# Performance work log

Measured on AMD Instinct MI355X. Metric: run time of the kernel, lower is better.

## Reference

```python
import jax, jax.numpy as jnp
import numpy as np

NHEAD = 16
HEAD_DIM = 64
EMBED_DIM = NHEAD * HEAD_DIM  # 1024
U, R, L, M = 2048, 256, 1024, 512


def setup_inputs() -> dict:
    key = jax.random.key(0)
    ks = jax.random.split(key, 11)
    D = EMBED_DIM
    inp = {
        "utterance": jax.random.normal(ks[0], (U, 1, D), jnp.float32),
        "right_context": jax.random.normal(ks[1], (R, 1, D), jnp.float32),
        "memory": jax.random.normal(ks[2], (M, 1, D), jnp.float32),
        "left_context_key": jax.random.normal(ks[3], (L, 1, D), jnp.float32),
        "left_context_val": jax.random.normal(ks[4], (L, 1, D), jnp.float32),
        "Wq": jax.random.normal(ks[5], (D, D), jnp.float32) * 0.02,
        "bq": jax.random.normal(ks[6], (D,), jnp.float32) * 0.02,
        "Wkv": jax.random.normal(ks[7], (2 * D, D), jnp.float32) * 0.02,
        "bkv": jax.random.normal(ks[8], (2 * D,), jnp.float32) * 0.02,
        "Wo": jax.random.normal(ks[9], (D, D), jnp.float32) * 0.02,
        "bo": jax.random.normal(ks[10], (D,), jnp.float32) * 0.02,
    }
    return inp


def reference(utterance, right_context, memory, left_context_key, left_context_val,
              Wq, bq, Wkv, bkv, Wo, bo):
    D = EMBED_DIM
    scaling = HEAD_DIM ** (-0.5)

    # query = Linear([right_context; utterance])  -> (Q, 1, D), Q = R + U
    q_in = jnp.concatenate([right_context, utterance], axis=0)
    query = q_in @ Wq.T + bq

    # key/value = Linear([memory; right_context; utterance]) split in two
    kv_in = jnp.concatenate([memory, right_context, utterance], axis=0)
    kv = kv_in @ Wkv.T + bkv  # (M+R+U, 1, 2D)
    k_new, v_new = kv[..., :D], kv[..., D:]

    # insert cached left-context key/value after [memory; right_context]
    key = jnp.concatenate([k_new[: M + R], left_context_key, k_new[M + R:]], axis=0)
    value = jnp.concatenate([v_new[: M + R], left_context_val, v_new[M + R:]], axis=0)

    Q = U + R
    KV = M + R + L + U
    # (T, 1, D) -> (nhead, T, head_dim)
    q = query.reshape(Q, NHEAD, HEAD_DIM).transpose(1, 0, 2)
    k = key.reshape(KV, NHEAD, HEAD_DIM).transpose(1, 0, 2)
    v = value.reshape(KV, NHEAD, HEAD_DIM).transpose(1, 0, 2)

    weights = jnp.einsum("hqd,hkd->hqk", q * scaling, k)  # (nhead, Q, KV)
    probs = jax.nn.softmax(weights, axis=-1)
    attn = jnp.einsum("hqk,hkd->hqd", probs, v)  # (nhead, Q, head_dim)

    attn = attn.transpose(1, 0, 2).reshape(Q, D)[:, None, :]  # (Q, 1, D)
    out = attn @ Wo.T + bo
    return out, key, value
```

## Files before the change

### kernel.cpp

```cpp
#include <hip/hip_runtime.h>
#include <hip/hip_bf16.h>

#define EMBED   1024
#define NHEADS  16
#define HDIM    64
#define U_LEN   2048
#define R_LEN   256
#define L_LEN   1024
#define M_LEN   512
#define Q_LEN   (U_LEN + R_LEN)
#define KV_LEN  (M_LEN + R_LEN + L_LEN + U_LEN)
#define X_ROWS  (M_LEN + R_LEN + U_LEN)
#define NPART   3
#define KV_PART (KV_LEN / NPART)

typedef __attribute__((ext_vector_type(8))) short short8;
typedef __attribute__((ext_vector_type(4))) float f32x4;
typedef __attribute__((ext_vector_type(16))) float f32x16;

#define QSCALE 0.180336880f

__device__ __forceinline__ void gl2lds16(const __hip_bfloat16* g, __hip_bfloat16* l) {
  __builtin_amdgcn_global_load_lds(
      (const __attribute__((address_space(1))) unsigned int*)g,
      (__attribute__((address_space(3))) unsigned int*)l, 16, 0, 0);
}

__device__ __forceinline__ unsigned pack_bf16(float a, float b) {
  unsigned r;
  asm("v_cvt_pk_bf16_f32 %0, %1, %2" : "=v"(r) : "v"(a), "v"(b));
  return r;
}

__device__ __forceinline__ void plane_swap(unsigned a, unsigned b, int h2,
                                           unsigned& lo, unsigned& hi) {
#if __has_builtin(__builtin_amdgcn_permlane32_swap)
  auto r = __builtin_amdgcn_permlane32_swap(a, b, false, false);
  lo = r[0]; hi = r[1];
#else
  unsigned s0 = h2 ? a : b;
  unsigned r0 = __shfl_xor(s0, 32, 64);
  lo = h2 ? r0 : a;
  hi = h2 ? b : r0;
#endif
}

__global__ __launch_bounds__(256) void prep_kernel(
    const float* __restrict__ mem, const float* __restrict__ rc,
    const float* __restrict__ utt, const float* __restrict__ lk,
    const float* __restrict__ lv, const float* __restrict__ Wq,
    const float* __restrict__ Wkv, const float* __restrict__ Wo,
    __hip_bfloat16* __restrict__ X, __hip_bfloat16* __restrict__ WB,
    __hip_bfloat16* __restrict__ WoB,
    float* __restrict__ key_out, float* __restrict__ val_out,
    __hip_bfloat16* __restrict__ k_bf, __hip_bfloat16* __restrict__ v_bf) {
  int b = blockIdx.x, tid = threadIdx.x;
  if (b < 2816) {
    int row = b, col = tid * 4;
    const float* src;
    if (row < M_LEN)              src = mem + row * EMBED;
    else if (row < M_LEN + R_LEN) src = rc + (row - M_LEN) * EMBED;
    else                          src = utt + (row - M_LEN - R_LEN) * EMBED;
    float4 v = *reinterpret_cast<const float4*>(src + col);
    uint2 pk; pk.x = pack_bf16(v.x, v.y); pk.y = pack_bf16(v.z, v.w);
    *reinterpret_cast<uint2*>(X + (size_t)row * EMBED + col) = pk;
  } else if (b < 6912) {
    const float* src; __hip_bfloat16* dst;
    int blk;
    if (b < 3840)      { src = Wq;  dst = WB;                blk = b - 2816; }
    else if (b < 5888) { src = Wkv; dst = WB + 1024 * 1024;  blk = b - 3840; }
    else               { src = Wo;  dst = WoB;               blk = b - 5888; }
    int idx = blk * 1024 + tid * 4;
    float4 v = *reinterpret_cast<const float4*>(src + idx);
    uint2 pk; pk.x = pack_bf16(v.x, v.y); pk.y = pack_bf16(v.z, v.w);
    *reinterpret_cast<uint2*>(dst + idx) = pk;
  } else {
    int row = b - 6912, c0 = tid * 4;
    int orow = 768 + row;
    float4 kv4 = *reinterpret_cast<const float4*>(lk + row * EMBED + c0);
    float4 vv4 = *reinterpret_cast<const float4*>(lv + row * EMBED + c0);
    *reinterpret_cast<float4*>(key_out + (size_t)orow * EMBED + c0) = kv4;
    *reinterpret_cast<float4*>(val_out + (size_t)orow * EMBED + c0) = vv4;
    uint2 pk, pv;
    pk.x = pack_bf16(kv4.x, kv4.y); pk.y = pack_bf16(kv4.z, kv4.w);
    pv.x = pack_bf16(vv4.x, vv4.y); pv.y = pack_bf16(vv4.z, vv4.w);
    *reinterpret_cast<uint2*>(k_bf + (size_t)orow * EMBED + c0) = pk;
    *reinterpret_cast<uint2*>(v_bf + (size_t)orow * EMBED + c0) = pv;
  }
}

__global__ __launch_bounds__(256) void transpose_kernel(
    const unsigned short* __restrict__ v_bf, unsigned short* __restrict__ vT) {
  __shared__ unsigned short T[64][72];
  int kt = blockIdx.x * 64, d0 = blockIdx.y * 64;
  int t = threadIdx.x;
  int r = t >> 3, c = (t & 7) * 8;
#pragma unroll
  for (int half = 0; half < 2; half++) {
    int kv = r + half * 32;
    short8 v = *reinterpret_cast<const short8*>(v_bf + (size_t)(kt + kv) * EMBED + d0 + c);
#pragma unroll
    for (int j = 0; j < 8; j++) T[c + j][kv] = (unsigned short)v[j];
  }
  __syncthreads();
#pragma unroll
  for (int half = 0; half < 2; half++) {
    int d = r + half * 32;
    *reinterpret_cast<short8*>(vT + (size_t)(d0 + d) * KV_LEN + kt + c) =
        *reinterpret_cast<const short8*>(&T[d][c]);
  }
}

__global__ __launch_bounds__(512) void gemm_qkv(
    const __hip_bfloat16* __restrict__ A, const __hip_bfloat16* __restrict__ B,
    const float* __restrict__ bq, const float* __restrict__ bkv,
    float* __restrict__ key_out, float* __restrict__ val_out,
    __hip_bfloat16* __restrict__ q_bf, __hip_bfloat16* __restrict__ k_bf,
    __hip_bfloat16* __restrict__ v_bf) {
  __shared__ __align__(16) __hip_bfloat16 As[128 * 64];
  __shared__ __align__(16) __hip_bfloat16 Bs[128 * 64];
  const int K = EMBED;
  int tid = threadIdx.x;
  int wave = tid >> 6, lane = tid & 63, quad = lane >> 4, l16 = lane & 15;
  int wm = wave >> 2, wn = wave & 3;
  int mbase = blockIdx.y * 128, nbase = blockIdx.x * 128;

  if (nbase + 128 <= 1024 && mbase + 128 <= 512) return;

  int srow = tid >> 3;
  int scol = ((tid & 7) ^ (srow & 7)) * 8;
  const __hip_bfloat16* aG = A + (size_t)(mbase + srow) * K + scol;
  const __hip_bfloat16* bG = B + (size_t)(nbase + srow) * K + scol;
  int swz = l16 & 7;

  f32x4 acc[4][2] = {};
  for (int kt = 0; kt < K; kt += 64) {
    gl2lds16(aG + kt, As + tid * 8);
    gl2lds16(aG + (size_t)64 * K + kt, As + (tid + 512) * 8);
    gl2lds16(bG + kt, Bs + tid * 8);
    gl2lds16(bG + (size_t)64 * K + kt, Bs + (tid + 512) * 8);
    __syncthreads();
#pragma unroll
    for (int ks = 0; ks < 2; ks++) {
      short8 af[4], bfr[2];
#pragma unroll
      for (int i = 0; i < 4; i++)
        af[i] = *reinterpret_cast<const short8*>(
            As + (wm * 64 + i * 16 + l16) * 64 + ((ks * 4 + quad) ^ swz) * 8);
#pragma unroll
      for (int j = 0; j < 2; j++)
        bfr[j] = *reinterpret_cast<const short8*>(
            Bs + (wn * 32 + j * 16 + l16) * 64 + ((ks * 4 + quad) ^ swz) * 8);
#pragma unroll
      for (int i = 0; i < 4; i++)
#pragma unroll
        for (int j = 0; j < 2; j++)
          acc[i][j] = __builtin_amdgcn_mfma_f32_16x16x32_bf16(af[i], bfr[j], acc[i][j], 0, 0, 0);
    }
    __syncthreads();
  }

#pragma unroll
  for (int i = 0; i < 4; i++) {
    int rb = mbase + wm * 64 + i * 16 + quad * 4;
#pragma unroll
    for (int j = 0; j < 2; j++) {
      int cg = nbase + wn * 32 + j * 16 + l16;
      float bv = (cg < 1024) ? bq[cg] : bkv[cg - 1024];
#pragma unroll
      for (int reg = 0; reg < 4; reg++) {
        int rg = rb + reg;
        float val = acc[i][j][reg] + bv;
        if (cg < 1024) {
          if (rg >= 512)
            q_bf[(size_t)(rg - 512) * 1024 + cg] = __float2bfloat16(val * QSCALE);
        } else {
          int orow = (rg < 768) ? rg : rg + 1024;
          if (cg < 2048) {
            int cc = cg - 1024;
            key_out[(size_t)orow * 1024 + cc] = val;
            k_bf[(size_t)orow * 1024 + cc] = __float2bfloat16(val);
          } else {
            int cc = cg - 2048;
            val_out[(size_t)orow * 1024 + cc] = val;
            v_bf[(size_t)orow * 1024 + cc] = __float2bfloat16(val);
          }
        }
      }
    }
  }
}

__global__ __launch_bounds__(256) void gemm_out(
    const __hip_bfloat16* __restrict__ A, const __hip_bfloat16* __restrict__ B,
    const float* __restrict__ bias, float* __restrict__ outf) {
  __shared__ __align__(16) __hip_bfloat16 As[64 * 64];
  __shared__ __align__(16) __hip_bfloat16 Bs[64 * 64];
  const int K = EMBED, N = EMBED;
  int tid = threadIdx.x;
  int wave = tid >> 6, lane = tid & 63, quad = lane >> 4, l16 = lane & 15;
  int wm = wave >> 1, wn = wave & 1;

  int lid = blockIdx.x;
  int gsw = (lid & 7) * 72 + (lid >> 3);
  int bx = gsw / 36, by = gsw % 36;
  int mbase = by * 64, nbase = bx * 64;

  int srow = tid >> 3;
  int scol = ((tid & 7) ^ (srow & 7)) * 8;
  const __hip_bfloat16* aG = A + (size_t)(mbase + srow) * K + scol;
  const __hip_bfloat16* bG = B + (size_t)(nbase + srow) * K + scol;
  int swz = l16 & 7;

  f32x4 acc[2][2] = {};
  for (int kt = 0; kt < K; kt += 64) {
    gl2lds16(aG + kt, As + tid * 8);
    gl2lds16(aG + (size_t)32 * K + kt, As + (tid + 256) * 8);
    gl2lds16(bG + kt, Bs + tid * 8);
    gl2lds16(bG + (size_t)32 * K + kt, Bs + (tid + 256) * 8);
    __syncthreads();
#pragma unroll
    for (int ks = 0; ks < 2; ks++) {
      short8 af[2], bfr[2];
#pragma unroll
      for (int i = 0; i < 2; i++)
        af[i] = *reinterpret_cast<const short8*>(
            As + (wm * 32 + i * 16 + l16) * 64 + ((ks * 4 + quad) ^ swz) * 8);
#pragma unroll
      for (int j = 0; j < 2; j++)
        bfr[j] = *reinterpret_cast<const short8*>(
            Bs + (wn * 32 + j * 16 + l16) * 64 + ((ks * 4 + quad) ^ swz) * 8);
#pragma unroll
      for (int i = 0; i < 2; i++)
#pragma unroll
        for (int j = 0; j < 2; j++)
          acc[i][j] = __builtin_amdgcn_mfma_f32_16x16x32_bf16(af[i], bfr[j], acc[i][j], 0, 0, 0);
    }
    __syncthreads();
  }

#pragma unroll
  for (int i = 0; i < 2; i++) {
    int rb = mbase + wm * 32 + i * 16 + quad * 4;
#pragma unroll
    for (int j = 0; j < 2; j++) {
      int cg = nbase + wn * 32 + j * 16 + l16;
      float bv = bias[cg];
#pragma unroll
      for (int reg = 0; reg < 4; reg++)
        outf[(size_t)(rb + reg) * N + cg] = acc[i][j][reg] + bv;
    }
  }
}

__global__ __launch_bounds__(256, 4) void attn_kernel(
    const __hip_bfloat16* __restrict__ q_bf, const __hip_bfloat16* __restrict__ k_bf,
    const __hip_bfloat16* __restrict__ vT,
    __hip_bfloat16* __restrict__ o_part, float* __restrict__ lsum) {
  __shared__ __align__(16) __hip_bfloat16 Ks[128][72];
  __shared__ __align__(16) __hip_bfloat16 VTs[64][136];
  int tid = threadIdx.x;
  int w = tid >> 6, lane = tid & 63, l31 = lane & 31, h2 = lane >> 5;

  int lid = blockIdx.x;
  int xcd = lid & 7, sfl = lid >> 3;
  int gi = sfl / 18, j = sfl - gi * 18;
  int g = gi * 8 + xcd;
  int part = g >> 4, h = g & 15;
  int qbase = j * 128;
  int qg = qbase + w * 32 + l31;

  short8 Qf[4];
#pragma unroll
  for (int ks = 0; ks < 4; ks++)
    Qf[ks] = *reinterpret_cast<const short8*>(
        q_bf + (size_t)qg * EMBED + h * HDIM + ks * 16 + h2 * 8);

  f32x16 ot[2] = {};
  float l_run = 0.f;

  int krow = tid >> 3, kcol = (tid & 7) * 8;
  int vrow = tid >> 4, vcol = (tid & 15) * 8;
  const int kv0 = part * KV_PART;

  short8 kr[4], vr[4];
#pragma unroll
  for (int v = 0; v < 4; v++) {
    kr[v] = *reinterpret_cast<const short8*>(
        k_bf + (size_t)(kv0 + v * 32 + krow) * EMBED + h * HDIM + kcol);
    vr[v] = *reinterpret_cast<const short8*>(
        vT + (size_t)(h * HDIM + v * 16 + vrow) * KV_LEN + kv0 + vcol);
  }

  for (int kt = kv0; kt < kv0 + KV_PART; kt += 128) {
    __syncthreads();
#pragma unroll
    for (int v = 0; v < 4; v++) {
      *reinterpret_cast<short8*>(&Ks[v * 32 + krow][kcol]) = kr[v];
      *reinterpret_cast<short8*>(&VTs[v * 16 + vrow][vcol]) = vr[v];
    }
    __syncthreads();
    if (kt + 128 < kv0 + KV_PART) {
#pragma unroll
      for (int v = 0; v < 4; v++) {
        kr[v] = *reinterpret_cast<const short8*>(
            k_bf + (size_t)(kt + 128 + v * 32 + krow) * EMBED + h * HDIM + kcol);
        vr[v] = *reinterpret_cast<const short8*>(
            vT + (size_t)(h * HDIM + v * 16 + vrow) * KV_LEN + kt + 128 + vcol);
      }
    }

#pragma unroll
    for (int kvs = 0; kvs < 4; kvs++) {
      f32x16 s = {};
      __builtin_amdgcn_s_setprio(1);
#pragma unroll
      for (int ks = 0; ks < 4; ks++) {
        short8 ak = *reinterpret_cast<const short8*>(&Ks[kvs * 32 + l31][ks * 16 + h2 * 8]);
        s = __builtin_amdgcn_mfma_f32_32x32x16_bf16(ak, Qf[ks], s, 0, 0, 0);
      }
      __builtin_amdgcn_s_setprio(0);
      unsigned u[4][2];
#pragma unroll
      for (int gq = 0; gq < 4; gq++) {
        float p0 = __builtin_amdgcn_exp2f(s[4 * gq + 0]);
        float p1 = __builtin_amdgcn_exp2f(s[4 * gq + 1]);
        float p2 = __builtin_amdgcn_exp2f(s[4 * gq + 2]);
        float p3 = __builtin_amdgcn_exp2f(s[4 * gq + 3]);
        l_run += (p0 + p1) + (p2 + p3);
        u[gq][0] = pack_bf16(p0, p1);
        u[gq][1] = pack_bf16(p2, p3);
      }
#pragma unroll
      for (int half = 0; half < 2; half++) {
        int c = kvs * 2 + half;
        int gA = 2 * half, gB = 2 * half + 1;
        uint4 fr;
        plane_swap(u[gA][0], u[gB][0], h2, fr.x, fr.z);
        plane_swap(u[gA][1], u[gB][1], h2, fr.y, fr.w);
        short8 pf = __builtin_bit_cast(short8, fr);
        __builtin_amdgcn_s_setprio(1);
#pragma unroll
        for (int ds = 0; ds < 2; ds++) {
          short8 av = *reinterpret_cast<const short8*>(&VTs[ds * 32 + l31][c * 16 + h2 * 8]);
          ot[ds] = __builtin_amdgcn_mfma_f32_32x32x16_bf16(av, pf, ot[ds], 0, 0, 0);
        }
        __builtin_amdgcn_s_setprio(0);
      }
    }
  }

  l_run += __shfl_xor(l_run, 32, 64);
  float inv = 1.0f / l_run;

  size_t orow = (size_t)part * Q_LEN + qg;
#pragma unroll
  for (int ds = 0; ds < 2; ds++)
#pragma unroll
    for (int gq = 0; gq < 4; gq++) {
      uint2 pk;
      pk.x = pack_bf16(ot[ds][4 * gq + 0] * inv, ot[ds][4 * gq + 1] * inv);
      pk.y = pack_bf16(ot[ds][4 * gq + 2] * inv, ot[ds][4 * gq + 3] * inv);
      *reinterpret_cast<uint2*>(
          o_part + orow * 1024 + h * HDIM + ds * 32 + gq * 8 + h2 * 4) = pk;
    }
  if (lane < 32)
    lsum[orow * NHEADS + h] = l_run;
}

__global__ __launch_bounds__(256) void merge_kernel(
    const __hip_bfloat16* __restrict__ o_part, const float* __restrict__ lsum,
    __hip_bfloat16* __restrict__ attn_bf) {
  int q = blockIdx.x;
  int c = threadIdx.x * 4;
  int h = c >> 6;
  float wt[NPART], L = 0.f;
#pragma unroll
  for (int p = 0; p < NPART; p++) {
    wt[p] = lsum[((size_t)p * Q_LEN + q) * NHEADS + h];
    L += wt[p];
  }
  float invL = 1.0f / L;
  float acc[4] = {0.f, 0.f, 0.f, 0.f};
#pragma unroll
  for (int p = 0; p < NPART; p++) {
    __hip_bfloat16 v[4];
    *reinterpret_cast<uint2*>(v) =
        *reinterpret_cast<const uint2*>(o_part + ((size_t)p * Q_LEN + q) * 1024 + c);
#pragma unroll
    for (int jj = 0; jj < 4; jj++) acc[jj] += wt[p] * __bfloat162float(v[jj]);
  }
  uint2 pk;
  pk.x = pack_bf16(acc[0] * invL, acc[1] * invL);
  pk.y = pack_bf16(acc[2] * invL, acc[3] * invL);
  *reinterpret_cast<uint2*>(attn_bf + (size_t)q * 1024 + c) = pk;
}


extern "C" void kernel_launch(void* const* d_in, const int* in_sizes, int n_in,
                              void* d_out, int out_size, void* d_ws, size_t ws_size,
                              hipStream_t stream) {
  const float* utt = (const float*)d_in[0];
  const float* rc  = (const float*)d_in[1];
  const float* mem = (const float*)d_in[2];
  const float* lk  = (const float*)d_in[3];
  const float* lv  = (const float*)d_in[4];
  const float* Wq  = (const float*)d_in[5];
  const float* bq  = (const float*)d_in[6];
  const float* Wkv = (const float*)d_in[7];
  const float* bkv = (const float*)d_in[8];
  const float* Wo  = (const float*)d_in[9];
  const float* bo  = (const float*)d_in[10];

  float* out_f   = (float*)d_out;
  float* key_out = out_f + Q_LEN * EMBED;
  float* val_out = key_out + KV_LEN * EMBED;

  char* ws = (char*)d_ws;
  size_t off = 0;
  __hip_bfloat16* X_bf   = (__hip_bfloat16*)(ws + off); off += (size_t)X_ROWS * EMBED * 2;
  __hip_bfloat16* WB_bf  = (__hip_bfloat16*)(ws + off); off += (size_t)3 * EMBED * EMBED * 2;
  __hip_bfloat16* Wo_bf  = (__hip_bfloat16*)(ws + off); off += (size_t)EMBED * EMBED * 2;
  __hip_bfloat16* q_bf   = (__hip_bfloat16*)(ws + off); off += (size_t)Q_LEN * EMBED * 2;
  __hip_bfloat16* k_bf   = (__hip_bfloat16*)(ws + off); off += (size_t)KV_LEN * EMBED * 2;
  __hip_bfloat16* vT_bf  = (__hip_bfloat16*)(ws + off); off += (size_t)EMBED * KV_LEN * 2;
  __hip_bfloat16* o_part = (__hip_bfloat16*)(ws + off); off += (size_t)NPART * Q_LEN * EMBED * 2;
  __hip_bfloat16* attn_bf = X_bf;
  float* lsum = (float*)WB_bf;
  __hip_bfloat16* v_bf = o_part;
  (void)off; (void)ws_size; (void)in_sizes; (void)n_in; (void)out_size;

  prep_kernel<<<7936, 256, 0, stream>>>(mem, rc, utt, lk, lv, Wq, Wkv, Wo,
                                        X_bf, WB_bf, Wo_bf,
                                        key_out, val_out, k_bf, v_bf);
  gemm_qkv<<<dim3(3 * EMBED / 128, X_ROWS / 128), 512, 0, stream>>>(
      X_bf, WB_bf, bq, bkv, key_out, val_out, q_bf, k_bf, v_bf);
  transpose_kernel<<<dim3(KV_LEN / 64, EMBED / 64), 256, 0, stream>>>(
      (const unsigned short*)v_bf, (unsigned short*)vT_bf);
  attn_kernel<<<dim3((Q_LEN / 128) * NHEADS * NPART), 256, 0, stream>>>(
      q_bf, k_bf, vT_bf, o_part, lsum);
  merge_kernel<<<Q_LEN, 256, 0, stream>>>(o_part, lsum, attn_bf);
  gemm_out<<<576, 256, 0, stream>>>(attn_bf, Wo_bf, bo, out_f);
}
```

Baseline: 200.8 us.

## Fuse V transpose into QKV GEMM epilogue and prep kernel

```diff
diff --git a/kernel.cpp b/kernel.cpp
--- a/kernel.cpp
+++ b/kernel.cpp
@@ -53,7 +53,7 @@
     __hip_bfloat16* __restrict__ X, __hip_bfloat16* __restrict__ WB,
     __hip_bfloat16* __restrict__ WoB,
     float* __restrict__ key_out, float* __restrict__ val_out,
-    __hip_bfloat16* __restrict__ k_bf, __hip_bfloat16* __restrict__ v_bf) {
+    __hip_bfloat16* __restrict__ k_bf, __hip_bfloat16* __restrict__ vT) {
   int b = blockIdx.x, tid = threadIdx.x;
   if (b < 2816) {
     int row = b, col = tid * 4;
@@ -74,40 +74,25 @@
     float4 v = *reinterpret_cast<const float4*>(src + idx);
     uint2 pk; pk.x = pack_bf16(v.x, v.y); pk.y = pack_bf16(v.z, v.w);
     *reinterpret_cast<uint2*>(dst + idx) = pk;
-  } else {
+  } else if (b < 7936) {
     int row = b - 6912, c0 = tid * 4;
     int orow = 768 + row;
     float4 kv4 = *reinterpret_cast<const float4*>(lk + row * EMBED + c0);
     float4 vv4 = *reinterpret_cast<const float4*>(lv + row * EMBED + c0);
     *reinterpret_cast<float4*>(key_out + (size_t)orow * EMBED + c0) = kv4;
     *reinterpret_cast<float4*>(val_out + (size_t)orow * EMBED + c0) = vv4;
-    uint2 pk, pv;
+    uint2 pk;
     pk.x = pack_bf16(kv4.x, kv4.y); pk.y = pack_bf16(kv4.z, kv4.w);
-    pv.x = pack_bf16(vv4.x, vv4.y); pv.y = pack_bf16(vv4.z, vv4.w);
     *reinterpret_cast<uint2*>(k_bf + (size_t)orow * EMBED + c0) = pk;
-    *reinterpret_cast<uint2*>(v_bf + (size_t)orow * EMBED + c0) = pv;
-  }
-}
-
-__global__ __launch_bounds__(256) void transpose_kernel(
-    const unsigned short* __restrict__ v_bf, unsigned short* __restrict__ vT) {
-  __shared__ unsigned short T[64][72];
-  int kt = blockIdx.x * 64, d0 = blockIdx.y * 64;
-  int t = threadIdx.x;
-  int r = t >> 3, c = (t & 7) * 8;
-#pragma unroll
-  for (int half = 0; half < 2; half++) {
-    int kv = r + half * 32;
-    short8 v = *reinterpret_cast<const short8*>(v_bf + (size_t)(kt + kv) * EMBED + d0 + c);
-#pragma unroll
-    for (int j = 0; j < 8; j++) T[c + j][kv] = (unsigned short)v[j];
-  }
-  __syncthreads();
-#pragma unroll
-  for (int half = 0; half < 2; half++) {
-    int d = r + half * 32;
-    *reinterpret_cast<short8*>(vT + (size_t)(d0 + d) * KV_LEN + kt + c) =
-        *reinterpret_cast<const short8*>(&T[d][c]);
+  } else {
+    int d = b - 7936;
+    int kv = tid * 4;
+    float v0 = lv[(size_t)(kv + 0) * EMBED + d];
+    float v1 = lv[(size_t)(kv + 1) * EMBED + d];
+    float v2 = lv[(size_t)(kv + 2) * EMBED + d];
+    float v3 = lv[(size_t)(kv + 3) * EMBED + d];
+    uint2 pk; pk.x = pack_bf16(v0, v1); pk.y = pack_bf16(v2, v3);
+    *reinterpret_cast<uint2*>(vT + (size_t)d * KV_LEN + 768 + kv) = pk;
   }
 }
 
@@ -116,7 +101,7 @@
     const float* __restrict__ bq, const float* __restrict__ bkv,
     float* __restrict__ key_out, float* __restrict__ val_out,
     __hip_bfloat16* __restrict__ q_bf, __hip_bfloat16* __restrict__ k_bf,
-    __hip_bfloat16* __restrict__ v_bf) {
+    __hip_bfloat16* __restrict__ vT) {
   __shared__ __align__(16) __hip_bfloat16 As[128 * 64];
   __shared__ __align__(16) __hip_bfloat16 Bs[128 * 64];
   const int K = EMBED;
@@ -167,24 +152,33 @@
     for (int j = 0; j < 2; j++) {
       int cg = nbase + wn * 32 + j * 16 + l16;
       float bv = (cg < 1024) ? bq[cg] : bkv[cg - 1024];
-#pragma unroll
-      for (int reg = 0; reg < 4; reg++) {
-        int rg = rb + reg;
-        float val = acc[i][j][reg] + bv;
-        if (cg < 1024) {
-          if (rg >= 512)
-            q_bf[(size_t)(rg - 512) * 1024 + cg] = __float2bfloat16(val * QSCALE);
+      float v0 = acc[i][j][0] + bv, v1 = acc[i][j][1] + bv;
+      float v2 = acc[i][j][2] + bv, v3 = acc[i][j][3] + bv;
+      if (cg < 1024) {
+        if (rb >= 512) {
+          __hip_bfloat16* qd = q_bf + (size_t)(rb - 512) * 1024 + cg;
+          qd[0]        = __float2bfloat16(v0 * QSCALE);
+          qd[1024]     = __float2bfloat16(v1 * QSCALE);
+          qd[2 * 1024] = __float2bfloat16(v2 * QSCALE);
+          qd[3 * 1024] = __float2bfloat16(v3 * QSCALE);
+        }
+      } else {
+        int orow = (rb < 768) ? rb : rb + 1024;
+        if (cg < 2048) {
+          int cc = cg - 1024;
+          float* kd = key_out + (size_t)orow * 1024 + cc;
+          kd[0] = v0; kd[1024] = v1; kd[2 * 1024] = v2; kd[3 * 1024] = v3;
+          __hip_bfloat16* kb = k_bf + (size_t)orow * 1024 + cc;
+          kb[0]        = __float2bfloat16(v0);
+          kb[1024]     = __float2bfloat16(v1);
+          kb[2 * 1024] = __float2bfloat16(v2);
+          kb[3 * 1024] = __float2bfloat16(v3);
         } else {
-          int orow = (rg < 768) ? rg : rg + 1024;
-          if (cg < 2048) {
-            int cc = cg - 1024;
-            key_out[(size_t)orow * 1024 + cc] = val;
-            k_bf[(size_t)orow * 1024 + cc] = __float2bfloat16(val);
-          } else {
-            int cc = cg - 2048;
-            val_out[(size_t)orow * 1024 + cc] = val;
-            v_bf[(size_t)orow * 1024 + cc] = __float2bfloat16(val);
-          }
+          int cc = cg - 2048;
+          float* vd = val_out + (size_t)orow * 1024 + cc;
+          vd[0] = v0; vd[1024] = v1; vd[2 * 1024] = v2; vd[3 * 1024] = v3;
+          uint2 pk; pk.x = pack_bf16(v0, v1); pk.y = pack_bf16(v2, v3);
+          *reinterpret_cast<uint2*>(vT + (size_t)cc * KV_LEN + orow) = pk;
         }
       }
     }
@@ -427,16 +421,13 @@
   __hip_bfloat16* o_part = (__hip_bfloat16*)(ws + off); off += (size_t)NPART * Q_LEN * EMBED * 2;
   __hip_bfloat16* attn_bf = X_bf;
   float* lsum = (float*)WB_bf;
-  __hip_bfloat16* v_bf = o_part;
   (void)off; (void)ws_size; (void)in_sizes; (void)n_in; (void)out_size;
 
-  prep_kernel<<<7936, 256, 0, stream>>>(mem, rc, utt, lk, lv, Wq, Wkv, Wo,
+  prep_kernel<<<8960, 256, 0, stream>>>(mem, rc, utt, lk, lv, Wq, Wkv, Wo,
                                         X_bf, WB_bf, Wo_bf,
-                                        key_out, val_out, k_bf, v_bf);
+                                        key_out, val_out, k_bf, vT_bf);
   gemm_qkv<<<dim3(3 * EMBED / 128, X_ROWS / 128), 512, 0, stream>>>(
-      X_bf, WB_bf, bq, bkv, key_out, val_out, q_bf, k_bf, v_bf);
-  transpose_kernel<<<dim3(KV_LEN / 64, EMBED / 64), 256, 0, stream>>>(
-      (const unsigned short*)v_bf, (unsigned short*)vT_bf);
+      X_bf, WB_bf, bq, bkv, key_out, val_out, q_bf, k_bf, vT_bf);
   attn_kernel<<<dim3((Q_LEN / 128) * NHEADS * NPART), 256, 0, stream>>>(
       q_bf, k_bf, vT_bf, o_part, lsum);
   merge_kernel<<<Q_LEN, 256, 0, stream>>>(o_part, lsum, attn_bf);
```

New measurement: 205.2 us. 2.2% more time.
